# Performance work log

Hardware: AMD Instinct MI355X
Metric: run time of the kernel (lower is better)

Reference implementation:

```python
import jax, jax.numpy as jnp
import numpy as np

EPS_SQRT = 1e-9
EPS_NORM = 1e-12


def setup_inputs() -> dict:
    key = jax.random.key(0)
    k1, k2 = jax.random.split(key)
    shape = (32, 112, 112, 128)  # B, H, W, C
    left = jax.random.normal(k1, shape, dtype=jnp.float32)
    right = jax.random.normal(k2, shape, dtype=jnp.float32)
    return {"left": left, "right": right}


def reference(left, right):
    B, H, W, C = left.shape
    # reshape to [B, H*W, C] and contract over the spatial dim -> [B, C, C]
    l = left.reshape(B, H * W, C)
    r = right.reshape(B, H * W, C)
    dotted = jnp.einsum('bxc,bxd->bcd', l, r)  # batched outer-product pooling
    flat = dotted.reshape(B, C * C)
    # signed square root
    sqrted = jnp.sign(flat) * jnp.sqrt(jnp.abs(flat) + EPS_SQRT)
    # L2 normalize over the flattened bilinear vector (tf.math.l2_normalize)
    sumsq = jnp.sum(jnp.square(sqrted), axis=-1, keepdims=True)
    normed = sqrted * jax.lax.rsqrt(jnp.maximum(sumsq, EPS_NORM))
    return normed
```

## Files before the change

### kernel.cpp

```cpp
#include <hip/hip_runtime.h>
#include <hip/hip_bf16.h>


#define NK      28
#define KC      448
#define BK      32
#define NSTEP   14
#define BATCH   32
#define CDIM    128
#define XDIM    12544

typedef __bf16 bf16x8 __attribute__((ext_vector_type(8)));
typedef float  f32x16 __attribute__((ext_vector_type(16)));

__device__ float g_part[(size_t)NK * BATCH * CDIM * CDIM];
__device__ float g_ssq[BATCH * 16];

__device__ __forceinline__ void split_pack(const float* f, uint4& hi, uint4& lo) {
  uint xh[8]; uint xl[8];
#pragma unroll
  for (int i = 0; i < 8; ++i) {
    uint u = __float_as_uint(f[i]);
    uint r = u + 0x7FFFu + ((u >> 16) & 1u);
    xh[i] = r;
    float hif = __uint_as_float(r & 0xFFFF0000u);
    xl[i] = __float_as_uint(f[i] - hif);
  }
  hi.x = __builtin_amdgcn_perm(xh[1], xh[0], 0x07060302u);
  hi.y = __builtin_amdgcn_perm(xh[3], xh[2], 0x07060302u);
  hi.z = __builtin_amdgcn_perm(xh[5], xh[4], 0x07060302u);
  hi.w = __builtin_amdgcn_perm(xh[7], xh[6], 0x07060302u);
  lo.x = __builtin_amdgcn_perm(xl[1], xl[0], 0x07060302u);
  lo.y = __builtin_amdgcn_perm(xl[3], xl[2], 0x07060302u);
  lo.z = __builtin_amdgcn_perm(xl[5], xl[4], 0x07060302u);
  lo.w = __builtin_amdgcn_perm(xl[7], xl[6], 0x07060302u);
}

__global__ __launch_bounds__(512, 2)
void bcnn_gemm_kernel(const float* __restrict__ L, const float* __restrict__ R) {
  const int chunk = blockIdx.x;
  const int b     = blockIdx.y;
  const int t     = threadIdx.x;
  const int l     = t & 63;
  const int w     = t >> 6;
  const int wr    = w >> 2;
  const int wc    = w & 3;
  const int lc    = l & 31;
  const int hh    = l >> 5;

  __shared__ uint4 sAhi[512];
  __shared__ uint4 sAlo[512];
  __shared__ uint4 sBhi[512];
  __shared__ uint4 sBlo[512];

  const int sc = t & 127;
  const int sh = t >> 7;
  const int wu = ((sc << 2) + sh) ^ ((sc >> 1) & 7);

  const size_t gofs = ((size_t)b * XDIM + (size_t)chunk * KC + sh * 8) * CDIM + sc;
  const float* Lp = L + gofs;
  const float* Rp = R + gofs;

  const int cA0 = wr * 64 + lc;
  const int cA1 = cA0 + 32;
  const int dB  = wc * 32 + lc;
  const int uA0 = ((cA0 << 2) + hh) ^ ((cA0 >> 1) & 7);
  const int uA1 = ((cA1 << 2) + hh) ^ ((cA1 >> 1) & 7);
  const int uB  = ((dB  << 2) + hh) ^ ((dB  >> 1) & 7);

  f32x16 acc0 = {};
  f32x16 acc1 = {};

  float fl[8], fr[8];
#pragma unroll
  for (int i = 0; i < 8; ++i) { fl[i] = Lp[i * CDIM]; fr[i] = Rp[i * CDIM]; }

  for (int s = 0; s < NSTEP; ++s) {
    __syncthreads();
    uint4 h4, l4;
    split_pack(fl, h4, l4);
    sAhi[wu] = h4; sAlo[wu] = l4;
    split_pack(fr, h4, l4);
    sBhi[wu] = h4; sBlo[wu] = l4;

    Lp = (s + 1 < NSTEP) ? Lp + BK * CDIM : L;
    Rp = (s + 1 < NSTEP) ? Rp + BK * CDIM : R;
#pragma unroll
    for (int i = 0; i < 8; ++i) { fl[i] = Lp[i * CDIM]; fr[i] = Rp[i * CDIM]; }

    __syncthreads();

#pragma unroll
    for (int ss = 0; ss < 2; ++ss) {
      const int x = ss << 1;
      bf16x8 ah0 = *(const bf16x8*)&sAhi[uA0 ^ x];
      bf16x8 al0 = *(const bf16x8*)&sAlo[uA0 ^ x];
      bf16x8 ah1 = *(const bf16x8*)&sAhi[uA1 ^ x];
      bf16x8 al1 = *(const bf16x8*)&sAlo[uA1 ^ x];
      bf16x8 bh  = *(const bf16x8*)&sBhi[uB  ^ x];
      bf16x8 bl  = *(const bf16x8*)&sBlo[uB  ^ x];
      acc0 = __builtin_amdgcn_mfma_f32_32x32x16_bf16(ah0, bh, acc0, 0, 0, 0);
      acc1 = __builtin_amdgcn_mfma_f32_32x32x16_bf16(ah1, bh, acc1, 0, 0, 0);
      acc0 = __builtin_amdgcn_mfma_f32_32x32x16_bf16(ah0, bl, acc0, 0, 0, 0);
      acc1 = __builtin_amdgcn_mfma_f32_32x32x16_bf16(ah1, bl, acc1, 0, 0, 0);
      acc0 = __builtin_amdgcn_mfma_f32_32x32x16_bf16(al0, bh, acc0, 0, 0, 0);
      acc1 = __builtin_amdgcn_mfma_f32_32x32x16_bf16(al1, bh, acc1, 0, 0, 0);
    }
  }

  float* outp = g_part + (((size_t)chunk * BATCH + b) << 14);
#pragma unroll
  for (int r = 0; r < 16; ++r) {
    const int row = (r & 3) + ((r >> 2) << 3) + (hh << 2);
    outp[(size_t)(wr * 64 + row) * CDIM + (wc * 32 + lc)]      = acc0[r];
    outp[(size_t)(wr * 64 + 32 + row) * CDIM + (wc * 32 + lc)] = acc1[r];
  }
}

__global__ void bcnn_sqrt_kernel(float* __restrict__ out) {
  const int b   = blockIdx.y;
  const int seg = blockIdx.x;
  const int t   = threadIdx.x;
  const int idx = seg * 1024 + t * 4;

  float4 v = {0.f, 0.f, 0.f, 0.f};
#pragma unroll
  for (int ch = 0; ch < NK; ++ch) {
    const float4 p = *(const float4*)&g_part[(((size_t)ch * BATCH + b) << 14) + idx];
    v.x += p.x; v.y += p.y; v.z += p.z; v.w += p.w;
  }
  float4 sv;
  {
    float a;
    a = sqrtf(fabsf(v.x) + 1e-9f); sv.x = (v.x > 0.f) ? a : ((v.x < 0.f) ? -a : 0.f);
    a = sqrtf(fabsf(v.y) + 1e-9f); sv.y = (v.y > 0.f) ? a : ((v.y < 0.f) ? -a : 0.f);
    a = sqrtf(fabsf(v.z) + 1e-9f); sv.z = (v.z > 0.f) ? a : ((v.z < 0.f) ? -a : 0.f);
    a = sqrtf(fabsf(v.w) + 1e-9f); sv.w = (v.w > 0.f) ? a : ((v.w < 0.f) ? -a : 0.f);
  }
  *(float4*)&out[((size_t)b << 14) + idx] = sv;

  float ss = sv.x * sv.x + sv.y * sv.y + sv.z * sv.z + sv.w * sv.w;
#pragma unroll
  for (int o = 32; o > 0; o >>= 1) ss += __shfl_down(ss, o, 64);
  __shared__ float red[4];
  if ((t & 63) == 0) red[t >> 6] = ss;
  __syncthreads();
  if (t == 0) g_ssq[b * 16 + seg] = red[0] + red[1] + red[2] + red[3];
}

__global__ void bcnn_scale_kernel(float* __restrict__ out) {
  const int b   = blockIdx.y;
  const int seg = blockIdx.x;
  const int t   = threadIdx.x;

  float tot = 0.f;
#pragma unroll
  for (int i = 0; i < 16; ++i) tot += g_ssq[b * 16 + i];
  const float scale = rsqrtf(fmaxf(tot, 1e-12f));

  const size_t base = ((size_t)b << 14) + seg * 1024 + t * 4;
  float4 v = *(float4*)&out[base];
  v.x *= scale; v.y *= scale; v.z *= scale; v.w *= scale;
  *(float4*)&out[base] = v;
}

extern "C" void kernel_launch(void* const* d_in, const int* in_sizes, int n_in,
                              void* d_out, int out_size, void* d_ws, size_t ws_size,
                              hipStream_t stream) {
  const float* L = (const float*)d_in[0];
  const float* R = (const float*)d_in[1];
  float* out = (float*)d_out;

  dim3 g1(NK, BATCH);
  bcnn_gemm_kernel<<<g1, 512, 0, stream>>>(L, R);

  dim3 g2(16, BATCH);
  bcnn_sqrt_kernel<<<g2, 256, 0, stream>>>(out);
  bcnn_scale_kernel<<<g2, 256, 0, stream>>>(out);
}
```

Before: 106.1 us.

## Stream raw fp32 tiles into LDS with async global_load_lds in a 4-stage pipeline

Replaces the register-staged load, split and LDS store with direct global-to-LDS async copies (global_load_lds) into a 4-deep ring buffer of raw fp32 tiles. The bf16 hi/lo split now happens after each wave reads from LDS, which means the same element is split redundantly by several waves. K-chunking changes from 28 chunks of 448 to 16 chunks of 784 with 16-row steps. This shrinks the grid and the partial-sum traffic. The pipeline is meant to hide global load latency behind MFMA work. The cost is more LDS reads, redundant conversion work, and unswizzled LDS access patterns that may cause bank conflicts.

```diff
diff --git a/kernel.cpp b/kernel.cpp
--- a/kernel.cpp
+++ b/kernel.cpp
@@ -2,10 +2,10 @@
 #include <hip/hip_bf16.h>
 
 
-#define NK      28
-#define KC      448
-#define BK      32
-#define NSTEP   14
+#define NK      16
+#define KC      784
+#define BK      16
+#define NT      49
 #define BATCH   32
 #define CDIM    128
 #define XDIM    12544
@@ -16,7 +16,7 @@
 __device__ float g_part[(size_t)NK * BATCH * CDIM * CDIM];
 __device__ float g_ssq[BATCH * 16];
 
-__device__ __forceinline__ void split_pack(const float* f, uint4& hi, uint4& lo) {
+__device__ __forceinline__ void split8(const float* f, uint4& hi, uint4& lo) {
   uint xh[8]; uint xl[8];
 #pragma unroll
   for (int i = 0; i < 8; ++i) {
@@ -38,6 +38,9 @@
 
 __global__ __launch_bounds__(512, 2)
 void bcnn_gemm_kernel(const float* __restrict__ L, const float* __restrict__ R) {
+  __shared__ float sL[4][BK * CDIM];
+  __shared__ float sR[4][BK * CDIM];
+
   const int chunk = blockIdx.x;
   const int b     = blockIdx.y;
   const int t     = threadIdx.x;
@@ -48,65 +51,75 @@
   const int lc    = l & 31;
   const int hh    = l >> 5;
 
-  __shared__ uint4 sAhi[512];
-  __shared__ uint4 sAlo[512];
-  __shared__ uint4 sBhi[512];
-  __shared__ uint4 sBlo[512];
-
-  const int sc = t & 127;
-  const int sh = t >> 7;
-  const int wu = ((sc << 2) + sh) ^ ((sc >> 1) & 7);
-
-  const size_t gofs = ((size_t)b * XDIM + (size_t)chunk * KC + sh * 8) * CDIM + sc;
-  const float* Lp = L + gofs;
-  const float* Rp = R + gofs;
+  const float* gL = L + ((size_t)b * XDIM + (size_t)chunk * KC) * CDIM + t * 4;
+  const float* gR = R + ((size_t)b * XDIM + (size_t)chunk * KC) * CDIM + t * 4;
 
   const int cA0 = wr * 64 + lc;
   const int cA1 = cA0 + 32;
   const int dB  = wc * 32 + lc;
-  const int uA0 = ((cA0 << 2) + hh) ^ ((cA0 >> 1) & 7);
-  const int uA1 = ((cA1 << 2) + hh) ^ ((cA1 >> 1) & 7);
-  const int uB  = ((dB  << 2) + hh) ^ ((dB  >> 1) & 7);
+  const int kbase = hh * 8 * CDIM;
 
   f32x16 acc0 = {};
   f32x16 acc1 = {};
 
-  float fl[8], fr[8];
-#pragma unroll
-  for (int i = 0; i < 8; ++i) { fl[i] = Lp[i * CDIM]; fr[i] = Rp[i * CDIM]; }
+#define STAGE(s)                                                                   \
+  do {                                                                             \
+    const float* pL_ = gL + (size_t)(s) * BK * CDIM;                               \
+    const float* pR_ = gR + (size_t)(s) * BK * CDIM;                               \
+    float* dL_ = &sL[(s) & 3][t * 4];                                              \
+    float* dR_ = &sR[(s) & 3][t * 4];                                              \
+    __builtin_amdgcn_global_load_lds(                                              \
+        (const __attribute__((address_space(1))) unsigned int*)pL_,                \
+        (__attribute__((address_space(3))) unsigned int*)dL_, 16, 0, 0);           \
+    __builtin_amdgcn_global_load_lds(                                              \
+        (const __attribute__((address_space(1))) unsigned int*)pR_,                \
+        (__attribute__((address_space(3))) unsigned int*)dR_, 16, 0, 0);           \
+  } while (0)
 
-  for (int s = 0; s < NSTEP; ++s) {
-    __syncthreads();
-    uint4 h4, l4;
-    split_pack(fl, h4, l4);
-    sAhi[wu] = h4; sAlo[wu] = l4;
-    split_pack(fr, h4, l4);
-    sBhi[wu] = h4; sBlo[wu] = l4;
+#define COMPUTE(s)                                                                 \
+  do {                                                                             \
+    const float* bufL_ = sL[(s) & 3];                                              \
+    const float* bufR_ = sR[(s) & 3];                                              \
+    float fA0[8], fA1[8], fB[8];                                                   \
+    _Pragma("unroll")                                                              \
+    for (int i = 0; i < 8; ++i) {                                                  \
+      fA0[i] = bufL_[kbase + i * CDIM + cA0];                                      \
+      fA1[i] = bufL_[kbase + i * CDIM + cA1];                                      \
+      fB[i]  = bufR_[kbase + i * CDIM + dB];                                       \
+    }                                                                              \
+    uint4 h0, l0, h1, l1, hb, lb;                                                  \
+    split8(fA0, h0, l0); split8(fA1, h1, l1); split8(fB, hb, lb);                  \
+    bf16x8 ah0 = *(bf16x8*)&h0, al0 = *(bf16x8*)&l0;                               \
+    bf16x8 ah1 = *(bf16x8*)&h1, al1 = *(bf16x8*)&l1;                               \
+    bf16x8 bh  = *(bf16x8*)&hb, bl  = *(bf16x8*)&lb;                               \
+    acc0 = __builtin_amdgcn_mfma_f32_32x32x16_bf16(ah0, bh, acc0, 0, 0, 0);        \
+    acc1 = __builtin_amdgcn_mfma_f32_32x32x16_bf16(ah1, bh, acc1, 0, 0, 0);        \
+    acc0 = __builtin_amdgcn_mfma_f32_32x32x16_bf16(ah0, bl, acc0, 0, 0, 0);        \
+    acc1 = __builtin_amdgcn_mfma_f32_32x32x16_bf16(ah1, bl, acc1, 0, 0, 0);        \
+    acc0 = __builtin_amdgcn_mfma_f32_32x32x16_bf16(al0, bh, acc0, 0, 0, 0);        \
+    acc1 = __builtin_amdgcn_mfma_f32_32x32x16_bf16(al1, bh, acc1, 0, 0, 0);        \
+  } while (0)
 
-    Lp = (s + 1 < NSTEP) ? Lp + BK * CDIM : L;
-    Rp = (s + 1 < NSTEP) ? Rp + BK * CDIM : R;
-#pragma unroll
-    for (int i = 0; i < 8; ++i) { fl[i] = Lp[i * CDIM]; fr[i] = Rp[i * CDIM]; }
+  STAGE(0); STAGE(1); STAGE(2);
 
-    __syncthreads();
+  for (int s = 0; s < NT - 2; ++s) {
+    asm volatile("s_waitcnt vmcnt(4) lgkmcnt(0)" ::: "memory");
+    __builtin_amdgcn_s_barrier();
+    asm volatile("" ::: "memory");
+    if (s + 3 < NT) STAGE(s + 3);
+    COMPUTE(s);
+  }
+  asm volatile("s_waitcnt vmcnt(2) lgkmcnt(0)" ::: "memory");
+  __builtin_amdgcn_s_barrier();
+  asm volatile("" ::: "memory");
+  COMPUTE(NT - 2);
+  asm volatile("s_waitcnt vmcnt(0) lgkmcnt(0)" ::: "memory");
+  __builtin_amdgcn_s_barrier();
+  asm volatile("" ::: "memory");
+  COMPUTE(NT - 1);
 
-#pragma unroll
-    for (int ss = 0; ss < 2; ++ss) {
-      const int x = ss << 1;
-      bf16x8 ah0 = *(const bf16x8*)&sAhi[uA0 ^ x];
-      bf16x8 al0 = *(const bf16x8*)&sAlo[uA0 ^ x];
-      bf16x8 ah1 = *(const bf16x8*)&sAhi[uA1 ^ x];
-      bf16x8 al1 = *(const bf16x8*)&sAlo[uA1 ^ x];
-      bf16x8 bh  = *(const bf16x8*)&sBhi[uB  ^ x];
-      bf16x8 bl  = *(const bf16x8*)&sBlo[uB  ^ x];
-      acc0 = __builtin_amdgcn_mfma_f32_32x32x16_bf16(ah0, bh, acc0, 0, 0, 0);
-      acc1 = __builtin_amdgcn_mfma_f32_32x32x16_bf16(ah1, bh, acc1, 0, 0, 0);
-      acc0 = __builtin_amdgcn_mfma_f32_32x32x16_bf16(ah0, bl, acc0, 0, 0, 0);
-      acc1 = __builtin_amdgcn_mfma_f32_32x32x16_bf16(ah1, bl, acc1, 0, 0, 0);
-      acc0 = __builtin_amdgcn_mfma_f32_32x32x16_bf16(al0, bh, acc0, 0, 0, 0);
-      acc1 = __builtin_amdgcn_mfma_f32_32x32x16_bf16(al1, bh, acc1, 0, 0, 0);
-    }
-  }
+#undef STAGE
+#undef COMPUTE
 
   float* outp = g_part + (((size_t)chunk * BATCH + b) << 14);
 #pragma unroll
```

Result: no change. 105.3 us (-0.8%).

## Double-buffer LDS with register prefetch, smaller k-step, fewer larger chunks

Applied to the files above, without the earlier changes.

Restructures the GEMM main loop to use two LDS buffer sets with one barrier per step, prefetching two steps of global data into registers so loads, the split/pack writes and MFMA compute overlap. The k-step drops from 32 to 16 rows, the number of K chunks goes from 28 to 16 (784 rows each), and the launch bound asks for 4 blocks per CU. This cuts per-step synchronisation and the partial-sum traffic in the reduction kernel, at the cost of fewer blocks in flight (512 instead of 896) and more loop iterations. The sqrt kernel still sums NK partials, so it follows the new chunk count.

```diff
diff --git a/kernel.cpp b/kernel.cpp
--- a/kernel.cpp
+++ b/kernel.cpp
@@ -2,10 +2,10 @@
 #include <hip/hip_bf16.h>
 
 
-#define NK      28
-#define KC      448
-#define BK      32
-#define NSTEP   14
+#define NK      16
+#define KC      784
+#define BK      16
+#define NT      49
 #define BATCH   32
 #define CDIM    128
 #define XDIM    12544
@@ -16,10 +16,10 @@
 __device__ float g_part[(size_t)NK * BATCH * CDIM * CDIM];
 __device__ float g_ssq[BATCH * 16];
 
-__device__ __forceinline__ void split_pack(const float* f, uint4& hi, uint4& lo) {
-  uint xh[8]; uint xl[8];
-#pragma unroll
-  for (int i = 0; i < 8; ++i) {
+__device__ __forceinline__ void split4(const float* f, uint2& hi, uint2& lo) {
+  uint xh[4], xl[4];
+#pragma unroll
+  for (int i = 0; i < 4; ++i) {
     uint u = __float_as_uint(f[i]);
     uint r = u + 0x7FFFu + ((u >> 16) & 1u);
     xh[i] = r;
@@ -28,16 +28,18 @@
   }
   hi.x = __builtin_amdgcn_perm(xh[1], xh[0], 0x07060302u);
   hi.y = __builtin_amdgcn_perm(xh[3], xh[2], 0x07060302u);
-  hi.z = __builtin_amdgcn_perm(xh[5], xh[4], 0x07060302u);
-  hi.w = __builtin_amdgcn_perm(xh[7], xh[6], 0x07060302u);
   lo.x = __builtin_amdgcn_perm(xl[1], xl[0], 0x07060302u);
   lo.y = __builtin_amdgcn_perm(xl[3], xl[2], 0x07060302u);
-  lo.z = __builtin_amdgcn_perm(xl[5], xl[4], 0x07060302u);
-  lo.w = __builtin_amdgcn_perm(xl[7], xl[6], 0x07060302u);
-}
-
-__global__ __launch_bounds__(512, 2)
+}
+
+__device__ __forceinline__ int ldsu(int c, int kh) {
+  return ((c << 1) | kh) ^ ((c >> 2) & 7);
+}
+
+__global__ __launch_bounds__(512, 4)
 void bcnn_gemm_kernel(const float* __restrict__ L, const float* __restrict__ R) {
+  __shared__ uint2 sAhi[2][512], sAlo[2][512], sBhi[2][512], sBlo[2][512];
+
   const int chunk = blockIdx.x;
   const int b     = blockIdx.y;
   const int t     = threadIdx.x;
@@ -48,65 +50,86 @@
   const int lc    = l & 31;
   const int hh    = l >> 5;
 
-  __shared__ uint4 sAhi[512];
-  __shared__ uint4 sAlo[512];
-  __shared__ uint4 sBhi[512];
-  __shared__ uint4 sBlo[512];
-
   const int sc = t & 127;
   const int sh = t >> 7;
-  const int wu = ((sc << 2) + sh) ^ ((sc >> 1) & 7);
-
-  const size_t gofs = ((size_t)b * XDIM + (size_t)chunk * KC + sh * 8) * CDIM + sc;
-  const float* Lp = L + gofs;
-  const float* Rp = R + gofs;
+  const int wslot = ldsu(sc, sh >> 1) * 2 + (sh & 1);
+
+  const float* gL = L + ((size_t)b * XDIM + (size_t)chunk * KC + sh * 4) * CDIM + sc;
+  const float* gR = R + ((size_t)b * XDIM + (size_t)chunk * KC + sh * 4) * CDIM + sc;
 
   const int cA0 = wr * 64 + lc;
   const int cA1 = cA0 + 32;
   const int dB  = wc * 32 + lc;
-  const int uA0 = ((cA0 << 2) + hh) ^ ((cA0 >> 1) & 7);
-  const int uA1 = ((cA1 << 2) + hh) ^ ((cA1 >> 1) & 7);
-  const int uB  = ((dB  << 2) + hh) ^ ((dB  >> 1) & 7);
+  const int uA0 = ldsu(cA0, hh) * 2;
+  const int uA1 = ldsu(cA1, hh) * 2;
+  const int uB  = ldsu(dB,  hh) * 2;
 
   f32x16 acc0 = {};
   f32x16 acc1 = {};
 
-  float fl[8], fr[8];
-#pragma unroll
-  for (int i = 0; i < 8; ++i) { fl[i] = Lp[i * CDIM]; fr[i] = Rp[i * CDIM]; }
-
-  for (int s = 0; s < NSTEP; ++s) {
-    __syncthreads();
-    uint4 h4, l4;
-    split_pack(fl, h4, l4);
-    sAhi[wu] = h4; sAlo[wu] = l4;
-    split_pack(fr, h4, l4);
-    sBhi[wu] = h4; sBlo[wu] = l4;
-
-    Lp = (s + 1 < NSTEP) ? Lp + BK * CDIM : L;
-    Rp = (s + 1 < NSTEP) ? Rp + BK * CDIM : R;
-#pragma unroll
-    for (int i = 0; i < 8; ++i) { fl[i] = Lp[i * CDIM]; fr[i] = Rp[i * CDIM]; }
-
-    __syncthreads();
-
-#pragma unroll
-    for (int ss = 0; ss < 2; ++ss) {
-      const int x = ss << 1;
-      bf16x8 ah0 = *(const bf16x8*)&sAhi[uA0 ^ x];
-      bf16x8 al0 = *(const bf16x8*)&sAlo[uA0 ^ x];
-      bf16x8 ah1 = *(const bf16x8*)&sAhi[uA1 ^ x];
-      bf16x8 al1 = *(const bf16x8*)&sAlo[uA1 ^ x];
-      bf16x8 bh  = *(const bf16x8*)&sBhi[uB  ^ x];
-      bf16x8 bl  = *(const bf16x8*)&sBlo[uB  ^ x];
-      acc0 = __builtin_amdgcn_mfma_f32_32x32x16_bf16(ah0, bh, acc0, 0, 0, 0);
-      acc1 = __builtin_amdgcn_mfma_f32_32x32x16_bf16(ah1, bh, acc1, 0, 0, 0);
-      acc0 = __builtin_amdgcn_mfma_f32_32x32x16_bf16(ah0, bl, acc0, 0, 0, 0);
-      acc1 = __builtin_amdgcn_mfma_f32_32x32x16_bf16(ah1, bl, acc1, 0, 0, 0);
-      acc0 = __builtin_amdgcn_mfma_f32_32x32x16_bf16(al0, bh, acc0, 0, 0, 0);
-      acc1 = __builtin_amdgcn_mfma_f32_32x32x16_bf16(al1, bh, acc1, 0, 0, 0);
-    }
-  }
+  float rlE[4], rrE[4], rlO[4], rrO[4];
+
+#define LOADR(rl, rr, s)                                                       \
+  do {                                                                         \
+    const float* pL_ = gL + (size_t)(s) * BK * CDIM;                           \
+    const float* pR_ = gR + (size_t)(s) * BK * CDIM;                           \
+    _Pragma("unroll")                                                          \
+    for (int i = 0; i < 4; ++i) { rl[i] = pL_[i * CDIM]; rr[i] = pR_[i * CDIM]; } \
+  } while (0)
+
+#define WRITE(rl, rr, set)                                                     \
+  do {                                                                         \
+    uint2 hi_, lo_;                                                            \
+    split4(rl, hi_, lo_);                                                      \
+    sAhi[set][wslot] = hi_; sAlo[set][wslot] = lo_;                            \
+    split4(rr, hi_, lo_);                                                      \
+    sBhi[set][wslot] = hi_; sBlo[set][wslot] = lo_;                            \
+  } while (0)
+
+#define COMPUTE(set)                                                           \
+  do {                                                                         \
+    bf16x8 ah0 = *(const bf16x8*)&sAhi[set][uA0];                              \
+    bf16x8 al0 = *(const bf16x8*)&sAlo[set][uA0];                              \
+    bf16x8 ah1 = *(const bf16x8*)&sAhi[set][uA1];                              \
+    bf16x8 al1 = *(const bf16x8*)&sAlo[set][uA1];                              \
+    bf16x8 bh  = *(const bf16x8*)&sBhi[set][uB];                               \
+    bf16x8 bl  = *(const bf16x8*)&sBlo[set][uB];                               \
+    acc0 = __builtin_amdgcn_mfma_f32_32x32x16_bf16(ah0, bh, acc0, 0, 0, 0);    \
+    acc1 = __builtin_amdgcn_mfma_f32_32x32x16_bf16(ah1, bh, acc1, 0, 0, 0);    \
+    acc0 = __builtin_amdgcn_mfma_f32_32x32x16_bf16(ah0, bl, acc0, 0, 0, 0);    \
+    acc1 = __builtin_amdgcn_mfma_f32_32x32x16_bf16(ah1, bl, acc1, 0, 0, 0);    \
+    acc0 = __builtin_amdgcn_mfma_f32_32x32x16_bf16(al0, bh, acc0, 0, 0, 0);    \
+    acc1 = __builtin_amdgcn_mfma_f32_32x32x16_bf16(al1, bh, acc1, 0, 0, 0);    \
+  } while (0)
+
+#define BAR()                                                                  \
+  do {                                                                         \
+    asm volatile("s_waitcnt lgkmcnt(0)" ::: "memory");                         \
+    __builtin_amdgcn_s_barrier();                                              \
+  } while (0)
+
+  LOADR(rlE, rrE, 0);
+  LOADR(rlO, rrO, 1);
+  WRITE(rlE, rrE, 0);
+  BAR();
+
+  for (int it = 0; it < 24; ++it) {
+    const int s0 = 2 * it;
+    LOADR(rlE, rrE, s0 + 2);
+    COMPUTE(0);
+    WRITE(rlO, rrO, 1);
+    BAR();
+    if (s0 + 3 < NT) LOADR(rlO, rrO, s0 + 3);
+    COMPUTE(1);
+    WRITE(rlE, rrE, 0);
+    BAR();
+  }
+  COMPUTE(0);
+
+#undef LOADR
+#undef WRITE
+#undef COMPUTE
+#undef BAR
 
   float* outp = g_part + (((size_t)chunk * BATCH + b) << 14);
 #pragma unroll
```

Result: faster. 96.18 us (-9.4%).

## Load GEMM operands straight into registers with triple-buffered prefetch, drop LDS staging

Applied to the files above, without the earlier changes.

The GEMM kernel no longer stages the split bf16 hi/lo operands through shared memory behind two barriers per step. Each lane now loads its own A and B columns directly from global memory into registers and rotates through three register buffers to keep loads in flight. The K chunk per block grows, cutting the number of partial-sum slabs from 28 to 8, which shrinks partial-buffer traffic and the reduction work in the sqrt kernel. In exchange, A and B columns are loaded and split redundantly by several waves, register pressure rises, and the grid drops to 256 blocks, which may reduce latency hiding.

```diff
diff --git a/kernel.cpp b/kernel.cpp
--- a/kernel.cpp
+++ b/kernel.cpp
@@ -2,10 +2,10 @@
 #include <hip/hip_bf16.h>
 
 
-#define NK      28
-#define KC      448
-#define BK      32
-#define NSTEP   14
+#define NK      8
+#define KC      1568
+#define KSTEP   16
+#define NT      98
 #define BATCH   32
 #define CDIM    128
 #define XDIM    12544
@@ -16,8 +16,8 @@
 __device__ float g_part[(size_t)NK * BATCH * CDIM * CDIM];
 __device__ float g_ssq[BATCH * 16];
 
-__device__ __forceinline__ void split_pack(const float* f, uint4& hi, uint4& lo) {
-  uint xh[8]; uint xl[8];
+__device__ __forceinline__ void split8(const float* f, uint4& hi, uint4& lo) {
+  uint xh[8], xl[8];
 #pragma unroll
   for (int i = 0; i < 8; ++i) {
     uint u = __float_as_uint(f[i]);
@@ -48,65 +48,70 @@
   const int lc    = l & 31;
   const int hh    = l >> 5;
 
-  __shared__ uint4 sAhi[512];
-  __shared__ uint4 sAlo[512];
-  __shared__ uint4 sBhi[512];
-  __shared__ uint4 sBlo[512];
-
-  const int sc = t & 127;
-  const int sh = t >> 7;
-  const int wu = ((sc << 2) + sh) ^ ((sc >> 1) & 7);
-
-  const size_t gofs = ((size_t)b * XDIM + (size_t)chunk * KC + sh * 8) * CDIM + sc;
-  const float* Lp = L + gofs;
-  const float* Rp = R + gofs;
-
   const int cA0 = wr * 64 + lc;
   const int cA1 = cA0 + 32;
-  const int dB  = wc * 32 + lc;
-  const int uA0 = ((cA0 << 2) + hh) ^ ((cA0 >> 1) & 7);
-  const int uA1 = ((cA1 << 2) + hh) ^ ((cA1 >> 1) & 7);
-  const int uB  = ((dB  << 2) + hh) ^ ((dB  >> 1) & 7);
+  const int cB  = wc * 32 + lc;
+
+  const size_t base = ((size_t)b * XDIM + (size_t)chunk * KC + hh * 8) * CDIM;
+  const float* pA0 = L + base + cA0;
+  const float* pA1 = L + base + cA1;
+  const float* pB  = R + base + cB;
+#define STEP_F (KSTEP * CDIM)
 
   f32x16 acc0 = {};
   f32x16 acc1 = {};
 
-  float fl[8], fr[8];
-#pragma unroll
-  for (int i = 0; i < 8; ++i) { fl[i] = Lp[i * CDIM]; fr[i] = Rp[i * CDIM]; }
+  float a0A[8], a1A[8], bA[8];
+  float a0B[8], a1B[8], bB[8];
+  float a0C[8], a1C[8], bC[8];
 
-  for (int s = 0; s < NSTEP; ++s) {
-    __syncthreads();
-    uint4 h4, l4;
-    split_pack(fl, h4, l4);
-    sAhi[wu] = h4; sAlo[wu] = l4;
-    split_pack(fr, h4, l4);
-    sBhi[wu] = h4; sBlo[wu] = l4;
+#define LOAD(a0, a1, bb)                                                        \
+  do {                                                                          \
+    _Pragma("unroll")                                                           \
+    for (int i = 0; i < 8; ++i) {                                               \
+      a0[i] = pA0[i * CDIM];                                                    \
+      a1[i] = pA1[i * CDIM];                                                    \
+      bb[i] = pB[i * CDIM];                                                     \
+    }                                                                           \
+    pA0 += STEP_F; pA1 += STEP_F; pB += STEP_F;                                 \
+  } while (0)
 
-    Lp = (s + 1 < NSTEP) ? Lp + BK * CDIM : L;
-    Rp = (s + 1 < NSTEP) ? Rp + BK * CDIM : R;
-#pragma unroll
-    for (int i = 0; i < 8; ++i) { fl[i] = Lp[i * CDIM]; fr[i] = Rp[i * CDIM]; }
+#define STEP(a0, a1, bb, PF)                                                    \
+  do {                                                                          \
+    uint4 h0_, l0_, h1_, l1_, hb_, lb_;                                         \
+    split8(a0, h0_, l0_);                                                       \
+    split8(a1, h1_, l1_);                                                       \
+    split8(bb, hb_, lb_);                                                       \
+    if (PF) LOAD(a0, a1, bb);                                                   \
+    bf16x8 ah0 = *(bf16x8*)&h0_, al0 = *(bf16x8*)&l0_;                          \
+    bf16x8 ah1 = *(bf16x8*)&h1_, al1 = *(bf16x8*)&l1_;                          \
+    bf16x8 bh  = *(bf16x8*)&hb_, bl  = *(bf16x8*)&lb_;                          \
+    acc0 = __builtin_amdgcn_mfma_f32_32x32x16_bf16(ah0, bh, acc0, 0, 0, 0);     \
+    acc1 = __builtin_amdgcn_mfma_f32_32x32x16_bf16(ah1, bh, acc1, 0, 0, 0);     \
+    acc0 = __builtin_amdgcn_mfma_f32_32x32x16_bf16(ah0, bl, acc0, 0, 0, 0);     \
+    acc1 = __builtin_amdgcn_mfma_f32_32x32x16_bf16(ah1, bl, acc1, 0, 0, 0);     \
+    acc0 = __builtin_amdgcn_mfma_f32_32x32x16_bf16(al0, bh, acc0, 0, 0, 0);     \
+    acc1 = __builtin_amdgcn_mfma_f32_32x32x16_bf16(al1, bh, acc1, 0, 0, 0);     \
+  } while (0)
 
-    __syncthreads();
+  LOAD(a0A, a1A, bA);
+  LOAD(a0B, a1B, bB);
+  LOAD(a0C, a1C, bC);
 
-#pragma unroll
-    for (int ss = 0; ss < 2; ++ss) {
-      const int x = ss << 1;
-      bf16x8 ah0 = *(const bf16x8*)&sAhi[uA0 ^ x];
-      bf16x8 al0 = *(const bf16x8*)&sAlo[uA0 ^ x];
-      bf16x8 ah1 = *(const bf16x8*)&sAhi[uA1 ^ x];
-      bf16x8 al1 = *(const bf16x8*)&sAlo[uA1 ^ x];
-      bf16x8 bh  = *(const bf16x8*)&sBhi[uB  ^ x];
-      bf16x8 bl  = *(const bf16x8*)&sBlo[uB  ^ x];
-      acc0 = __builtin_amdgcn_mfma_f32_32x32x16_bf16(ah0, bh, acc0, 0, 0, 0);
-      acc1 = __builtin_amdgcn_mfma_f32_32x32x16_bf16(ah1, bh, acc1, 0, 0, 0);
-      acc0 = __builtin_amdgcn_mfma_f32_32x32x16_bf16(ah0, bl, acc0, 0, 0, 0);
-      acc1 = __builtin_amdgcn_mfma_f32_32x32x16_bf16(ah1, bl, acc1, 0, 0, 0);
-      acc0 = __builtin_amdgcn_mfma_f32_32x32x16_bf16(al0, bh, acc0, 0, 0, 0);
-      acc1 = __builtin_amdgcn_mfma_f32_32x32x16_bf16(al1, bh, acc1, 0, 0, 0);
-    }
+  for (int it = 0; it < 31; ++it) {
+    STEP(a0A, a1A, bA, 1);
+    STEP(a0B, a1B, bB, 1);
+    STEP(a0C, a1C, bC, 1);
   }
+  STEP(a0A, a1A, bA, 1);
+  STEP(a0B, a1B, bB, 1);
+  STEP(a0C, a1C, bC, 0);
+  STEP(a0A, a1A, bA, 0);
+  STEP(a0B, a1B, bB, 0);
+
+#undef LOAD
+#undef STEP
+#undef STEP_F
 
   float* outp = g_part + (((size_t)chunk * BATCH + b) << 14);
 #pragma unroll
```

Measured after the change: 108.6 us. 1.02x slower.
